# Performance work log

Hardware: AMD Instinct MI355X
Metric: run time of the kernel (lower is better)

The kernel has to match this reference:

```python
import jax, jax.numpy as jnp
import numpy as np

N = 10000
D_IN = 256
D_OUT = 128


def setup_inputs() -> dict:
    key = jax.random.key(0)
    ks = jax.random.split(key, 8)
    H_k = jax.random.normal(ks[0], (N, D_IN), dtype=jnp.float32)
    A = (jax.random.uniform(ks[1], (N, N)) < 0.003).astype(jnp.float32)
    W_w = jax.random.normal(ks[2], (D_OUT, D_IN), dtype=jnp.float32) * (1.0 / np.sqrt(D_IN))
    W_b = jax.random.normal(ks[3], (D_OUT,), dtype=jnp.float32) * 0.01
    vkt_w = jax.random.normal(ks[4], (1, D_OUT), dtype=jnp.float32) * (1.0 / np.sqrt(D_OUT))
    vkt_b = jax.random.normal(ks[5], (1,), dtype=jnp.float32) * 0.01
    vkr_w = jax.random.normal(ks[6], (1, D_OUT), dtype=jnp.float32) * (1.0 / np.sqrt(D_OUT))
    vkr_b = jax.random.normal(ks[7], (1,), dtype=jnp.float32) * 0.01
    return {"H_k": H_k, "A": A, "W_w": W_w, "W_b": W_b,
            "vkt_w": vkt_w, "vkt_b": vkt_b, "vkr_w": vkr_w, "vkr_b": vkr_b}


def reference(H_k, A, W_w, W_b, vkt_w, vkt_b, vkr_w, vkr_b):
    WH = jax.nn.relu(H_k @ W_w.T + W_b)            # [N, D_OUT]
    s = WH @ vkt_w.T + vkt_b                        # [N, 1] sender scores
    r = WH @ vkr_w.T + vkr_b                        # [N, 1] receiver scores
    # M_s[i,j] = A[i,j] * s[j] ; M_r = (A * r.T).T  => M_r[i,j] = A[j,i] * r[i]
    M = A * s.reshape(1, N) + A.T * r.reshape(N, 1)  # [N, N]
    # torch F.softmax with no dim on a 2D tensor -> softmax over dim=1
    Attention = jax.nn.softmax(jax.nn.sigmoid(M), axis=1)
    return Attention @ WH                            # [N, D_OUT]
```

## Files before the change

kernel.cpp:

```cpp
#include <hip/hip_runtime.h>
#include <math.h>

#define N 10000
#define DIN 256
#define DOUT 128
#define CAP 192
#define MAXP 400000
#define LBUF 2048
#define C0 1.6487212707001282f

__global__ __launch_bounds__(256) void k_gemm(
        const float* __restrict__ H, const float* __restrict__ W,
        const float* __restrict__ Wb,
        const float* __restrict__ vt, const float* __restrict__ vtb,
        const float* __restrict__ vr, const float* __restrict__ vrb,
        float* __restrict__ WH, float* __restrict__ s_out, float* __restrict__ r_out,
        int* __restrict__ rowcount, float* __restrict__ colsum, int* __restrict__ gcnt)
{
    __shared__ float hs[32 * 260];
    __shared__ float wt[64 * 132];
    const int t = threadIdx.x;
    const int brow = blockIdx.x * 32;

    {
        if (t < 32) {
            int idx = blockIdx.x * 32 + t;
            if (idx < N) rowcount[idx] = 0;
        }
        if (blockIdx.x == 0) {
            if (t < DOUT) colsum[t] = 0.f;
            if (t == 255) gcnt[0] = 0;
        }
    }

    #pragma unroll
    for (int l = 0; l < 8; ++l) {
        int fid = t + l * 256;
        int row = fid >> 6;
        int f4  = fid & 63;
        int grow = brow + row;
        float4 v = make_float4(0.f, 0.f, 0.f, 0.f);
        if (grow < N) v = *(const float4*)(H + (size_t)grow * DIN + f4 * 4);
        *(float4*)(hs + row * 260 + f4 * 4) = v;
    }

    float acc[4][4];
    #pragma unroll
    for (int i = 0; i < 4; ++i)
        #pragma unroll
        for (int j = 0; j < 4; ++j) acc[i][j] = 0.f;

    const int tx = t & 31;
    const int ty = t >> 5;

    for (int kc = 0; kc < 4; ++kc) {
        __syncthreads();
        #pragma unroll
        for (int l = 0; l < 8; ++l) {
            int fid = t + l * 256;
            int col = fid >> 4;
            int kq  = fid & 15;
            float4 v = *(const float4*)(W + (size_t)col * DIN + kc * 64 + kq * 4);
            wt[(kq * 4 + 0) * 132 + col] = v.x;
            wt[(kq * 4 + 1) * 132 + col] = v.y;
            wt[(kq * 4 + 2) * 132 + col] = v.z;
            wt[(kq * 4 + 3) * 132 + col] = v.w;
        }
        __syncthreads();
        #pragma unroll 4
        for (int k = 0; k < 64; ++k) {
            float4 w4 = *(const float4*)(wt + k * 132 + tx * 4);
            int gk = kc * 64 + k;
            float h0 = hs[(ty * 4 + 0) * 260 + gk];
            float h1 = hs[(ty * 4 + 1) * 260 + gk];
            float h2 = hs[(ty * 4 + 2) * 260 + gk];
            float h3 = hs[(ty * 4 + 3) * 260 + gk];
            acc[0][0] += h0 * w4.x; acc[0][1] += h0 * w4.y; acc[0][2] += h0 * w4.z; acc[0][3] += h0 * w4.w;
            acc[1][0] += h1 * w4.x; acc[1][1] += h1 * w4.y; acc[1][2] += h1 * w4.z; acc[1][3] += h1 * w4.w;
            acc[2][0] += h2 * w4.x; acc[2][1] += h2 * w4.y; acc[2][2] += h2 * w4.z; acc[2][3] += h2 * w4.w;
            acc[3][0] += h3 * w4.x; acc[3][1] += h3 * w4.y; acc[3][2] += h3 * w4.z; acc[3][3] += h3 * w4.w;
        }
    }

    __syncthreads();
    float4 bias = *(const float4*)(Wb + tx * 4);
    #pragma unroll
    for (int i = 0; i < 4; ++i) {
        int row = ty * 4 + i;
        int grow = brow + row;
        float4 o;
        o.x = fmaxf(acc[i][0] + bias.x, 0.f);
        o.y = fmaxf(acc[i][1] + bias.y, 0.f);
        o.z = fmaxf(acc[i][2] + bias.z, 0.f);
        o.w = fmaxf(acc[i][3] + bias.w, 0.f);
        *(float4*)(wt + row * 132 + tx * 4) = o;
        if (grow < N) *(float4*)(WH + (size_t)grow * DOUT + tx * 4) = o;
    }
    __syncthreads();

    const int wv = t >> 6, ln = t & 63;
    float vt0 = vt[2 * ln], vt1 = vt[2 * ln + 1];
    float vr0 = vr[2 * ln], vr1 = vr[2 * ln + 1];
    for (int rr = 0; rr < 8; ++rr) {
        int row = wv * 8 + rr;
        float a = wt[row * 132 + 2 * ln];
        float b = wt[row * 132 + 2 * ln + 1];
        float sp = a * vt0 + b * vt1;
        float rp = a * vr0 + b * vr1;
        #pragma unroll
        for (int off = 32; off; off >>= 1) {
            sp += __shfl_xor(sp, off);
            rp += __shfl_xor(rp, off);
        }
        int grow = brow + row;
        if (ln == 0 && grow < N) {
            s_out[grow] = sp + vtb[0];
            r_out[grow] = rp + vrb[0];
        }
    }
}

__global__ __launch_bounds__(256) void k_scan(const float* __restrict__ A,
        const float* __restrict__ WH,
        unsigned* __restrict__ pairs, int* __restrict__ gcnt,
        float* __restrict__ colsum)
{
    __shared__ unsigned pbuf[LBUF];
    __shared__ int pcnt;
    __shared__ int gbase;
    if (threadIdx.x == 0) pcnt = 0;
    __syncthreads();

    if (blockIdx.x < 79) {
        int col = threadIdx.x & 127;
        int rbase = blockIdx.x * 128 + (threadIdx.x >> 7);
        float cs = 0.f;
        #pragma unroll 4
        for (int k = 0; k < 64; ++k) {
            int row = rbase + 2 * k;
            if (row < N) cs += WH[(size_t)row * DOUT + col];
        }
        atomicAdd(&colsum[col], cs);
    }

    const uint4* Au = (const uint4*)A;
    const size_t stride = (size_t)gridDim.x * blockDim.x;
    const size_t total4 = (size_t)N * (size_t)N / 4;
    size_t i = (size_t)blockIdx.x * blockDim.x + threadIdx.x;

#define PUSH(E) do { \
        int pos_ = atomicAdd(&pcnt, 1); \
        if (pos_ < LBUF) pbuf[pos_] = (E); \
        else { int gp_ = atomicAdd(gcnt, 1); if (gp_ < MAXP) pairs[gp_] = (E); } \
    } while (0)

#define SCAN_BODY(I) do { \
        uint4 v_ = Au[I]; \
        if (v_.x | v_.y | v_.z | v_.w) { \
            unsigned eb_ = (unsigned)((I) * 4); \
            if (v_.x) PUSH(eb_); \
            if (v_.y) PUSH(eb_ + 1); \
            if (v_.z) PUSH(eb_ + 2); \
            if (v_.w) PUSH(eb_ + 3); \
        } } while (0)

    for (; i + stride < total4; i += 2 * stride) {
        SCAN_BODY(i);
        SCAN_BODY(i + stride);
    }
    for (; i < total4; i += stride) SCAN_BODY(i);
#undef SCAN_BODY
#undef PUSH

    __syncthreads();
    int cnt = pcnt; if (cnt > LBUF) cnt = LBUF;
    if (threadIdx.x == 0 && cnt > 0) gbase = atomicAdd(gcnt, cnt);
    __syncthreads();
    if (cnt > 0) {
        int base = gbase;
        for (int k = threadIdx.x; k < cnt; k += 256) {
            int gp = base + k;
            if (gp < MAXP) pairs[gp] = pbuf[k];
        }
    }
}

__global__ __launch_bounds__(256) void k_build(const unsigned* __restrict__ pairs,
        const int* __restrict__ gcnt, int* __restrict__ rowcount,
        unsigned* __restrict__ rowdata)
{
    int npair = gcnt[0]; if (npair > MAXP) npair = MAXP;
    int tid = blockIdx.x * 256 + threadIdx.x;
    if (tid >= npair) return;
    unsigned e = pairs[tid];
    unsigned p = e / (unsigned)N;
    unsigned q = e - p * (unsigned)N;
    int pos = atomicAdd(&rowcount[p], 1);
    if (pos < CAP) rowdata[(size_t)p * CAP + pos] = q;
    int pos2 = atomicAdd(&rowcount[q], 1);
    if (pos2 < CAP) rowdata[(size_t)q * CAP + pos2] = p | 0x8000u;
}

__global__ __launch_bounds__(256) void k_out(const float* __restrict__ WH,
        const float* __restrict__ s, const float* __restrict__ r,
        const float* __restrict__ colsum, const int* __restrict__ rowcount,
        const unsigned* __restrict__ rowdata, float* __restrict__ out)
{
    __shared__ unsigned ent[4][CAP];
    __shared__ float del[4][CAP];
    const int wv = threadIdx.x >> 6, ln = threadIdx.x & 63;
    const int row = blockIdx.x * 4 + wv;
    int n = rowcount[row]; if (n > CAP) n = CAP;
    const float rrow = r[row];

    unsigned my[3]; int myslot[3]; int nslots = 0;
    for (int slot = ln; slot < n; slot += 64) {
        unsigned e = rowdata[(size_t)row * CAP + slot];
        ent[wv][slot] = e;
        my[nslots] = e; myslot[nslots] = slot; nslots++;
    }
    __syncthreads();

    bool addr_[3] = {false, false, false}, dead[3] = {false, false, false};
    for (int j = 0; j < n; ++j) {
        unsigned bc = ent[wv][j];
        #pragma unroll
        for (int k = 0; k < 3; ++k) {
            if (k < nslots && myslot[k] != j) {
                unsigned mine = my[k];
                if (((mine ^ bc) & 0x8000u) && ((mine & 0x3FFFu) == (bc & 0x3FFFu))) {
                    if (mine & 0x8000u) dead[k] = true;
                    else addr_[k] = true;
                }
            }
        }
    }

    float zpart = 0.f;
    #pragma unroll
    for (int k = 0; k < 3; ++k) {
        if (k < nslots) {
            float dlt = 0.f;
            if (!dead[k]) {
                unsigned col = my[k] & 0x3FFFu;
                float m = (my[k] & 0x8000u) ? rrow : s[col];
                if (addr_[k]) m += rrow;
                float sg = 1.f / (1.f + __expf(-m));
                dlt = expf(sg) - C0;
            }
            del[wv][myslot[k]] = dlt;
            zpart += dlt;
        }
    }
    #pragma unroll
    for (int off = 32; off; off >>= 1) zpart += __shfl_xor(zpart, off);
    __syncthreads();

    float acc0 = 0.f, acc1 = 0.f;
    for (int e2 = 0; e2 < n; ++e2) {
        float dlt = del[wv][e2];
        if (dlt != 0.f) {
            unsigned col = ent[wv][e2] & 0x3FFFu;
            float2 w2 = *(const float2*)(WH + (size_t)col * DOUT + 2 * ln);
            acc0 += dlt * w2.x;
            acc1 += dlt * w2.y;
        }
    }
    float inv = 1.f / (C0 * (float)N + zpart);
    int d = 2 * ln;
    out[(size_t)row * DOUT + d]     = (C0 * colsum[d]     + acc0) * inv;
    out[(size_t)row * DOUT + d + 1] = (C0 * colsum[d + 1] + acc1) * inv;
}

extern "C" void kernel_launch(void* const* d_in, const int* in_sizes, int n_in,
                              void* d_out, int out_size, void* d_ws, size_t ws_size,
                              hipStream_t stream)
{
    (void)in_sizes; (void)n_in; (void)out_size; (void)ws_size;
    const float* H   = (const float*)d_in[0];
    const float* A   = (const float*)d_in[1];
    const float* W   = (const float*)d_in[2];
    const float* Wb  = (const float*)d_in[3];
    const float* vt  = (const float*)d_in[4];
    const float* vtb = (const float*)d_in[5];
    const float* vr  = (const float*)d_in[6];
    const float* vrb = (const float*)d_in[7];

    char* ws = (char*)d_ws;
    size_t off = 0;
    float* WH = (float*)(ws + off);        off += (size_t)N * DOUT * 4;
    float* s_ = (float*)(ws + off);        off += 40960;
    float* r_ = (float*)(ws + off);        off += 40960;
    float* colsum = (float*)(ws + off);    off += 1024;
    int* rowcount = (int*)(ws + off);      off += 40960;
    int* gcnt = (int*)(ws + off);          off += 256;
    unsigned* pairs = (unsigned*)(ws + off); off += (size_t)MAXP * 4;
    unsigned* rowdata = (unsigned*)(ws + off);

    k_gemm<<<(N + 31) / 32, 256, 0, stream>>>(H, W, Wb, vt, vtb, vr, vrb,
                                              WH, s_, r_, rowcount, colsum, gcnt);
    k_scan<<<2048, 256, 0, stream>>>(A, WH, pairs, gcnt, colsum);
    k_build<<<(MAXP + 255) / 256, 256, 0, stream>>>(pairs, gcnt, rowcount, rowdata);
    k_out<<<N / 4, 256, 0, stream>>>(WH, s_, r_, colsum, rowcount, rowdata, (float*)d_out);
}
```

Baseline: 300.4 us.

## Fuse adjacency list build into scan kernel and precompute column sums in GEMM

Removes the separate pair buffer and k_build kernel. The scan kernel now inserts nonzeros directly into the per-row adjacency lists, first staging them in shared memory. Column sums of WH are computed as per-block partials inside the GEMM epilogue and reduced by one block in the scan, replacing the reread of WH with atomics. The A scan uses nontemporal 4-way unrolled loads to raise memory-level parallelism on the 400MB stream. This saves a launch and a global round trip for the pairs, at the cost of more atomics inside the bandwidth-bound scan.

```diff
diff --git a/kernel.cpp b/kernel.cpp
--- a/kernel.cpp
+++ b/kernel.cpp
@@ -5,9 +5,11 @@
 #define DIN 256
 #define DOUT 128
 #define CAP 192
-#define MAXP 400000
-#define LBUF 2048
+#define LBUF 1024
+#define NGB 313
 #define C0 1.6487212707001282f
+
+typedef unsigned int u32x4 __attribute__((ext_vector_type(4)));
 
 __global__ __launch_bounds__(256) void k_gemm(
         const float* __restrict__ H, const float* __restrict__ W,
@@ -15,22 +17,16 @@
         const float* __restrict__ vt, const float* __restrict__ vtb,
         const float* __restrict__ vr, const float* __restrict__ vrb,
         float* __restrict__ WH, float* __restrict__ s_out, float* __restrict__ r_out,
-        int* __restrict__ rowcount, float* __restrict__ colsum, int* __restrict__ gcnt)
+        int* __restrict__ rowcount, float* __restrict__ cspart)
 {
     __shared__ float hs[32 * 260];
     __shared__ float wt[64 * 132];
     const int t = threadIdx.x;
     const int brow = blockIdx.x * 32;
 
-    {
-        if (t < 32) {
-            int idx = blockIdx.x * 32 + t;
-            if (idx < N) rowcount[idx] = 0;
-        }
-        if (blockIdx.x == 0) {
-            if (t < DOUT) colsum[t] = 0.f;
-            if (t == 255) gcnt[0] = 0;
-        }
+    if (t < 32) {
+        int idx = brow + t;
+        if (idx < N) rowcount[idx] = 0;
     }
 
     #pragma unroll
@@ -118,87 +114,84 @@
             r_out[grow] = rp + vrb[0];
         }
     }
+
+    if (t < 128) {
+        float cs = 0.f;
+        int nvalid = N - brow; if (nvalid > 32) nvalid = 32;
+        for (int rr = 0; rr < nvalid; ++rr) cs += wt[rr * 132 + t];
+        cspart[(size_t)blockIdx.x * 128 + t] = cs;
+    }
 }
 
 __global__ __launch_bounds__(256) void k_scan(const float* __restrict__ A,
-        const float* __restrict__ WH,
-        unsigned* __restrict__ pairs, int* __restrict__ gcnt,
-        float* __restrict__ colsum)
+        const float* __restrict__ cspart, float* __restrict__ colsum,
+        int* __restrict__ rowcount, unsigned* __restrict__ rowdata)
 {
     __shared__ unsigned pbuf[LBUF];
     __shared__ int pcnt;
-    __shared__ int gbase;
     if (threadIdx.x == 0) pcnt = 0;
     __syncthreads();
 
-    if (blockIdx.x < 79) {
-        int col = threadIdx.x & 127;
-        int rbase = blockIdx.x * 128 + (threadIdx.x >> 7);
+    if (blockIdx.x == 0 && threadIdx.x < 128) {
         float cs = 0.f;
-        #pragma unroll 4
-        for (int k = 0; k < 64; ++k) {
-            int row = rbase + 2 * k;
-            if (row < N) cs += WH[(size_t)row * DOUT + col];
-        }
-        atomicAdd(&colsum[col], cs);
-    }
-
-    const uint4* Au = (const uint4*)A;
-    const size_t stride = (size_t)gridDim.x * blockDim.x;
+        for (int b = 0; b < NGB; ++b) cs += cspart[(size_t)b * 128 + threadIdx.x];
+        colsum[threadIdx.x] = cs;
+    }
+
+    const u32x4* Au = (const u32x4*)A;
+    const size_t s1 = (size_t)gridDim.x * blockDim.x;
     const size_t total4 = (size_t)N * (size_t)N / 4;
     size_t i = (size_t)blockIdx.x * blockDim.x + threadIdx.x;
 
 #define PUSH(E) do { \
         int pos_ = atomicAdd(&pcnt, 1); \
         if (pos_ < LBUF) pbuf[pos_] = (E); \
-        else { int gp_ = atomicAdd(gcnt, 1); if (gp_ < MAXP) pairs[gp_] = (E); } \
+        else {  \
+            unsigned p_ = (E) / (unsigned)N, q_ = (E) - p_ * (unsigned)N; \
+            int a_ = atomicAdd(&rowcount[p_], 1); \
+            if (a_ < CAP) rowdata[(size_t)p_ * CAP + a_] = q_; \
+            int b_ = atomicAdd(&rowcount[q_], 1); \
+            if (b_ < CAP) rowdata[(size_t)q_ * CAP + b_] = p_ | 0x8000u; \
+        } \
     } while (0)
 
-#define SCAN_BODY(I) do { \
-        uint4 v_ = Au[I]; \
-        if (v_.x | v_.y | v_.z | v_.w) { \
+#define BODY(V, I) do { \
+        if ((V).x | (V).y | (V).z | (V).w) { \
             unsigned eb_ = (unsigned)((I) * 4); \
-            if (v_.x) PUSH(eb_); \
-            if (v_.y) PUSH(eb_ + 1); \
-            if (v_.z) PUSH(eb_ + 2); \
-            if (v_.w) PUSH(eb_ + 3); \
+            if ((V).x) PUSH(eb_); \
+            if ((V).y) PUSH(eb_ + 1); \
+            if ((V).z) PUSH(eb_ + 2); \
+            if ((V).w) PUSH(eb_ + 3); \
         } } while (0)
 
-    for (; i + stride < total4; i += 2 * stride) {
-        SCAN_BODY(i);
-        SCAN_BODY(i + stride);
-    }
-    for (; i < total4; i += stride) SCAN_BODY(i);
-#undef SCAN_BODY
+    for (; i + 3 * s1 < total4; i += 4 * s1) {
+        u32x4 v0 = __builtin_nontemporal_load(Au + i);
+        u32x4 v1 = __builtin_nontemporal_load(Au + i + s1);
+        u32x4 v2 = __builtin_nontemporal_load(Au + i + 2 * s1);
+        u32x4 v3 = __builtin_nontemporal_load(Au + i + 3 * s1);
+        BODY(v0, i);
+        BODY(v1, i + s1);
+        BODY(v2, i + 2 * s1);
+        BODY(v3, i + 3 * s1);
+    }
+    for (; i < total4; i += s1) {
+        u32x4 v = __builtin_nontemporal_load(Au + i);
+        BODY(v, i);
+    }
+#undef BODY
 #undef PUSH
 
     __syncthreads();
     int cnt = pcnt; if (cnt > LBUF) cnt = LBUF;
-    if (threadIdx.x == 0 && cnt > 0) gbase = atomicAdd(gcnt, cnt);
-    __syncthreads();
-    if (cnt > 0) {
-        int base = gbase;
-        for (int k = threadIdx.x; k < cnt; k += 256) {
-            int gp = base + k;
-            if (gp < MAXP) pairs[gp] = pbuf[k];
-        }
-    }
-}
-
-__global__ __launch_bounds__(256) void k_build(const unsigned* __restrict__ pairs,
-        const int* __restrict__ gcnt, int* __restrict__ rowcount,
-        unsigned* __restrict__ rowdata)
-{
-    int npair = gcnt[0]; if (npair > MAXP) npair = MAXP;
-    int tid = blockIdx.x * 256 + threadIdx.x;
-    if (tid >= npair) return;
-    unsigned e = pairs[tid];
-    unsigned p = e / (unsigned)N;
-    unsigned q = e - p * (unsigned)N;
-    int pos = atomicAdd(&rowcount[p], 1);
-    if (pos < CAP) rowdata[(size_t)p * CAP + pos] = q;
-    int pos2 = atomicAdd(&rowcount[q], 1);
-    if (pos2 < CAP) rowdata[(size_t)q * CAP + pos2] = p | 0x8000u;
+    for (int k = threadIdx.x; k < cnt; k += 256) {
+        unsigned e = pbuf[k];
+        unsigned p = e / (unsigned)N;
+        unsigned q = e - p * (unsigned)N;
+        int pos = atomicAdd(&rowcount[p], 1);
+        if (pos < CAP) rowdata[(size_t)p * CAP + pos] = q;
+        int pos2 = atomicAdd(&rowcount[q], 1);
+        if (pos2 < CAP) rowdata[(size_t)q * CAP + pos2] = p | 0x8000u;
+    }
 }
 
 __global__ __launch_bounds__(256) void k_out(const float* __restrict__ WH,
@@ -292,14 +285,12 @@
     float* s_ = (float*)(ws + off);        off += 40960;
     float* r_ = (float*)(ws + off);        off += 40960;
     float* colsum = (float*)(ws + off);    off += 1024;
+    float* cspart = (float*)(ws + off);    off += (size_t)NGB * 128 * 4;
     int* rowcount = (int*)(ws + off);      off += 40960;
-    int* gcnt = (int*)(ws + off);          off += 256;
-    unsigned* pairs = (unsigned*)(ws + off); off += (size_t)MAXP * 4;
     unsigned* rowdata = (unsigned*)(ws + off);
 
-    k_gemm<<<(N + 31) / 32, 256, 0, stream>>>(H, W, Wb, vt, vtb, vr, vrb,
-                                              WH, s_, r_, rowcount, colsum, gcnt);
-    k_scan<<<2048, 256, 0, stream>>>(A, WH, pairs, gcnt, colsum);
-    k_build<<<(MAXP + 255) / 256, 256, 0, stream>>>(pairs, gcnt, rowcount, rowdata);
+    k_gemm<<<NGB, 256, 0, stream>>>(H, W, Wb, vt, vtb, vr, vrb,
+                                    WH, s_, r_, rowcount, cspart);
+    k_scan<<<2048, 256, 0, stream>>>(A, cspart, colsum, rowcount, rowdata);
     k_out<<<N / 4, 256, 0, stream>>>(WH, s_, r_, colsum, rowcount, rowdata, (float*)d_out);
 }
```

New measurement: 269.3 us. -10.4%, faster.
